# Kernel optimization log

Measured on AMD Instinct MI355X. Metric: run time of the kernel, lower is better.

The kernel has to match this reference:

```python
import jax, jax.numpy as jnp
import numpy as np

B, S, E, L, H, FF, CB = 16, 1000, 512, 4, 8, 2048, 4096
DH = E // H

def _ln(x, g, b):
    m = x.mean(-1, keepdims=True)
    v = ((x - m) ** 2).mean(-1, keepdims=True)
    return (x - m) / jnp.sqrt(v + 1e-5) * g + b

def setup_inputs() -> dict:
    key = jax.random.key(0)
    cnt = [0]
    def rn(shape, s=0.02):
        cnt[0] += 1
        return jax.random.normal(jax.random.fold_in(key, cnt[0]), shape, jnp.float32) * s
    inp = {}
    inp['noisy_tokens'] = jax.random.randint(jax.random.fold_in(key, 999), (B, S), 0, CB, dtype=jnp.int32)
    inp['codebook'] = rn((CB, E), 1.0)
    # sinusoidal positional encoding, as in _create_positional_encoding
    pe = np.zeros((S, E), np.float32)
    pos = np.arange(S, dtype=np.float32)[:, None]
    div = np.exp(np.arange(0, E, 2, dtype=np.float32) * (-np.log(10000.0) / E))
    pe[:, 0::2] = np.sin(pos * div)
    pe[:, 1::2] = np.cos(pos * div)
    inp['pos_enc'] = jnp.asarray(pe)[None]  # [1,S,E]
    # transformer encoder layers (stacked over L)
    inp['qkv_w'] = rn((L, 3 * E, E)); inp['qkv_b'] = jnp.zeros((L, 3 * E))
    inp['out_w'] = rn((L, E, E));     inp['out_b'] = jnp.zeros((L, E))
    inp['ln1_g'] = jnp.ones((L, E));  inp['ln1_b'] = jnp.zeros((L, E))
    inp['ln2_g'] = jnp.ones((L, E));  inp['ln2_b'] = jnp.zeros((L, E))
    inp['ff1_w'] = rn((L, FF, E));    inp['ff1_b'] = jnp.zeros((L, FF))
    inp['ff2_w'] = rn((L, E, FF));    inp['ff2_b'] = jnp.zeros((L, E))
    inp['fin_g'] = jnp.ones((E,));    inp['fin_b'] = jnp.zeros((E,))
    # post_process: Linear, LN, GELU, Linear
    inp['pp1_w'] = rn((E, E)); inp['pp1_b'] = jnp.zeros((E,))
    inp['pp_ln_g'] = jnp.ones((E,)); inp['pp_ln_b'] = jnp.zeros((E,))
    inp['pp2_w'] = rn((E, E)); inp['pp2_b'] = jnp.zeros((E,))
    inp['res_w'] = jnp.float32(0.1)
    # feature_to_codebook: Linear, LN, GELU, Linear (codebook_dim == E)
    inp['fc1_w'] = rn((E, E)); inp['fc1_b'] = jnp.zeros((E,))
    inp['fc_ln_g'] = jnp.ones((E,)); inp['fc_ln_b'] = jnp.zeros((E,))
    inp['fc2_w'] = rn((E, E)); inp['fc2_b'] = jnp.zeros((E,))
    return inp

def reference(noisy_tokens, codebook, pos_enc, qkv_w, qkv_b, out_w, out_b,
              ln1_g, ln1_b, ln2_g, ln2_b, ff1_w, ff1_b, ff2_w, ff2_b,
              fin_g, fin_b, pp1_w, pp1_b, pp_ln_g, pp_ln_b, pp2_w, pp2_b,
              res_w, fc1_w, fc1_b, fc_ln_g, fc_ln_b, fc2_w, fc2_b):
    gelu = lambda z: jax.nn.gelu(z, approximate=False)
    # token embedding (codebook_projection is Identity) + positional encoding
    x = codebook[noisy_tokens] + pos_enc            # [B,S,E]
    # pre-norm transformer encoder (dropout=0 / eval)
    y = x
    for l in range(L):
        h = _ln(y, ln1_g[l], ln1_b[l])
        qkv = h @ qkv_w[l].T + qkv_b[l]             # [B,S,3E]
        q, k, v = jnp.split(qkv, 3, axis=-1)
        q = q.reshape(B, S, H, DH); k = k.reshape(B, S, H, DH); v = v.reshape(B, S, H, DH)
        scores = jnp.einsum('bqhd,bkhd->bhqk', q, k) / jnp.sqrt(jnp.float32(DH))
        attn = jax.nn.softmax(scores, axis=-1)
        ctx = jnp.einsum('bhqk,bkhd->bqhd', attn, v).reshape(B, S, E)
        y = y + (ctx @ out_w[l].T + out_b[l])
        h2 = _ln(y, ln2_g[l], ln2_b[l])
        y = y + (gelu(h2 @ ff1_w[l].T + ff1_b[l]) @ ff2_w[l].T + ff2_b[l])
    y = _ln(y, fin_g, fin_b)
    # post_process + residual
    pp = gelu(_ln(y @ pp1_w.T + pp1_b, pp_ln_g, pp_ln_b)) @ pp2_w.T + pp2_b
    enhanced = x + res_w * pp
    # feature_to_codebook
    fc = gelu(_ln(enhanced @ fc1_w.T + fc1_b, fc_ln_g, fc_ln_b)) @ fc2_w.T + fc2_b  # [B,S,E]
    # quantize: nearest neighbour in codebook (cdist + argmin)
    flat = fc.reshape(-1, E)
    d2 = (jnp.sum(flat ** 2, -1, keepdims=True)
          - 2.0 * flat @ codebook.T
          + jnp.sum(codebook ** 2, -1))            # [B*S, CB]
    tokens = jnp.argmin(d2, axis=-1).reshape(B, S)
    return fc, tokens
```

## Files before the change

### kernel.cpp

```cpp
#include <hip/hip_runtime.h>
#include <hip/hip_bf16.h>
#include <math.h>

#define NTOK 16000
#define E    512
#define FFD  2048
#define CBN  4096
#define SEQ  1000
#define NH   8
#define VLD  1008

typedef __hip_bfloat16 bf16;
typedef __attribute__((ext_vector_type(8))) short short8;
typedef __attribute__((ext_vector_type(4))) float f32x4;

__device__ __forceinline__ float gelu_f(float v) {
    return 0.5f * v * (1.0f + erff(v * 0.70710678118654752f));
}

__device__ __forceinline__ void split_store(float v, bf16* hi, bf16* lo, size_t idx) {
    bf16 h = __float2bfloat16(v);
    hi[idx] = h;
    lo[idx] = __float2bfloat16(v - __bfloat162float(h));
}

__device__ __forceinline__ void gll16(const bf16* g, short* l) {
    __builtin_amdgcn_global_load_lds((const __attribute__((address_space(1))) void*)g,
                                     (__attribute__((address_space(3))) void*)l, 16, 0, 0);
}

__device__ __forceinline__ void t2_ins(float v, int c, float& v1, int& c1, float& v2, int& c2) {
    const bool b1 = (v < v1) || (v == v1 && c < c1);
    const bool b2 = (v < v2) || (v == v2 && c < c2);
    if (b1) { v2 = v1; c2 = c1; v1 = v; c1 = c; }
    else if (b2) { v2 = v; c2 = c; }
}

__global__ __launch_bounds__(128) void embed_kernel(const int* __restrict__ tok,
                                                    const float* __restrict__ cb,
                                                    const float* __restrict__ pe,
                                                    float* __restrict__ y) {
    const int row = blockIdx.x;
    const int s = row % SEQ;
    const int t = tok[row];
    const int c = threadIdx.x * 4;
    const float4 cv = *(const float4*)(cb + (size_t)t * E + c);
    const float4 pv = *(const float4*)(pe + (size_t)s * E + c);
    *(float4*)(y + (size_t)row * E + c) =
        make_float4(cv.x + pv.x, cv.y + pv.y, cv.z + pv.z, cv.w + pv.w);
}

__global__ __launch_bounds__(256) void split_w(const float* __restrict__ src, int ld,
                                               int cols_log2, int n,
                                               bf16* __restrict__ hi, bf16* __restrict__ lo) {
    const int i = blockIdx.x * 256 + threadIdx.x;
    if (i >= n) return;
    const int r = i >> cols_log2;
    const int c = i & ((1 << cols_log2) - 1);
    const float v = src[(size_t)r * ld + c];
    split_store(v, hi, lo, i);
}

template<int GELU>
__global__ __launch_bounds__(256) void ln_planes(const float* __restrict__ in,
                                                 bf16* __restrict__ hi, bf16* __restrict__ lo,
                                                 const float* __restrict__ g,
                                                 const float* __restrict__ b) {
    const int lane = threadIdx.x & 63;
    const int row = blockIdx.x * 4 + (threadIdx.x >> 6);
    const float* p = in + (size_t)row * E;
    const float4 v0 = *(const float4*)(p + lane * 4);
    const float4 v1 = *(const float4*)(p + 256 + lane * 4);
    float sum = v0.x + v0.y + v0.z + v0.w + v1.x + v1.y + v1.z + v1.w;
    float sq = v0.x * v0.x + v0.y * v0.y + v0.z * v0.z + v0.w * v0.w
             + v1.x * v1.x + v1.y * v1.y + v1.z * v1.z + v1.w * v1.w;
#pragma unroll
    for (int m = 1; m < 64; m <<= 1) {
        sum += __shfl_xor(sum, m);
        sq += __shfl_xor(sq, m);
    }
    const float mean = sum * (1.0f / 512.0f);
    const float var = sq * (1.0f / 512.0f) - mean * mean;
    const float rstd = rsqrtf(var + 1e-5f);
    const float4 g0 = *(const float4*)(g + lane * 4);
    const float4 g1 = *(const float4*)(g + 256 + lane * 4);
    const float4 b0 = *(const float4*)(b + lane * 4);
    const float4 b1 = *(const float4*)(b + 256 + lane * 4);
    const size_t base = (size_t)row * E;
    float o;
    const float vv0[4] = {v0.x, v0.y, v0.z, v0.w};
    const float gg0[4] = {g0.x, g0.y, g0.z, g0.w};
    const float bb0[4] = {b0.x, b0.y, b0.z, b0.w};
    const float vv1[4] = {v1.x, v1.y, v1.z, v1.w};
    const float gg1[4] = {g1.x, g1.y, g1.z, g1.w};
    const float bb1[4] = {b1.x, b1.y, b1.z, b1.w};
#pragma unroll
    for (int t = 0; t < 4; ++t) {
        o = (vv0[t] - mean) * rstd * gg0[t] + bb0[t];
        if (GELU) o = gelu_f(o);
        split_store(o, hi, lo, base + lane * 4 + t);
        o = (vv1[t] - mean) * rstd * gg1[t] + bb1[t];
        if (GELU) o = gelu_f(o);
        split_store(o, hi, lo, base + 256 + lane * 4 + t);
    }
}

template<int OUT>
__global__ __launch_bounds__(256) void gemm_split(
    const bf16* __restrict__ Ah, const bf16* __restrict__ Al, int lda,
    const bf16* __restrict__ Wh, const bf16* __restrict__ Wl, int ldw,
    const float* __restrict__ bias,
    float* __restrict__ C, int ldc,
    bf16* __restrict__ Ohi, bf16* __restrict__ Olo, int ldp,
    const int* __restrict__ noisy, const float* __restrict__ cb,
    const float* __restrict__ pe, const float* __restrict__ resw,
    int K) {
    __shared__ __align__(16) short SB[2][4][128][32];
    const int tid = threadIdx.x;
    const int rowBase = blockIdx.y * 128;
    const int colBase = blockIdx.x * 128;
    const int wave = tid >> 6, lane = tid & 63;
    const int wm = (wave & 1) * 64, wn = (wave >> 1) * 64;
    const int lm = lane & 15;
    const int psl8 = ((lane >> 4) ^ ((lm >> 1) & 3)) * 8;

    const bf16* src = (wave == 0) ? Ah : (wave == 1) ? Al : (wave == 2) ? Wh : Wl;
    const int sld = (wave < 2) ? lda : ldw;
    const int srb = (wave < 2) ? rowBase : colBase;
    const int sslot = (lane & 3) ^ ((lane >> 3) & 3);
    const bf16* sp = src + (size_t)(srb + (lane >> 2)) * sld + sslot * 8;
    short* lb0 = &SB[0][wave][0][0];
    short* lb1 = &SB[1][wave][0][0];

    f32x4 acc[4][4];
#pragma unroll
    for (int i = 0; i < 4; ++i)
#pragma unroll
        for (int j = 0; j < 4; ++j)
            acc[i][j] = (f32x4){0.f, 0.f, 0.f, 0.f};

    const int nt = K >> 5;
#pragma unroll
    for (int j = 0; j < 8; ++j)
        gll16(sp + (size_t)j * 16 * sld, lb0 + j * 512);
    {
        const bf16* p = sp + 32;
#pragma unroll
        for (int j = 0; j < 8; ++j)
            gll16(p + (size_t)j * 16 * sld, lb1 + j * 512);
    }
    for (int t = 0; t < nt; ++t) {
        const int cur = t & 1;
        if (t + 1 < nt) asm volatile("s_waitcnt vmcnt(8)" ::: "memory");
        else            asm volatile("s_waitcnt vmcnt(0)" ::: "memory");
        __builtin_amdgcn_s_barrier();
        __builtin_amdgcn_sched_barrier(0);
        const short (*P)[128][32] = SB[cur];
        short8 ah[4], al[4], wh[4], wl[4];
#pragma unroll
        for (int i = 0; i < 4; ++i) {
            ah[i] = *(const short8*)&P[0][wm + i * 16 + lm][psl8];
            al[i] = *(const short8*)&P[1][wm + i * 16 + lm][psl8];
            wh[i] = *(const short8*)&P[2][wn + i * 16 + lm][psl8];
            wl[i] = *(const short8*)&P[3][wn + i * 16 + lm][psl8];
        }
#pragma unroll
        for (int i = 0; i < 4; ++i)
#pragma unroll
            for (int j = 0; j < 4; ++j)
                acc[i][j] = __builtin_amdgcn_mfma_f32_16x16x32_bf16(ah[i], wh[j], acc[i][j], 0, 0, 0);
#pragma unroll
        for (int i = 0; i < 4; ++i)
#pragma unroll
            for (int j = 0; j < 4; ++j)
                acc[i][j] = __builtin_amdgcn_mfma_f32_16x16x32_bf16(ah[i], wl[j], acc[i][j], 0, 0, 0);
#pragma unroll
        for (int i = 0; i < 4; ++i)
#pragma unroll
            for (int j = 0; j < 4; ++j)
                acc[i][j] = __builtin_amdgcn_mfma_f32_16x16x32_bf16(al[i], wh[j], acc[i][j], 0, 0, 0);
        __builtin_amdgcn_s_barrier();
        if (t + 2 < nt) {
            short* lb = cur ? lb1 : lb0;
            const bf16* p = sp + (t + 2) * 32;
#pragma unroll
            for (int j = 0; j < 8; ++j)
                gll16(p + (size_t)j * 16 * sld, lb + j * 512);
        }
    }

    float bv[4];
#pragma unroll
    for (int j = 0; j < 4; ++j)
        bv[j] = bias ? bias[colBase + wn + j * 16 + lm] : 0.f;
    float scv = 0.f;
    if (OUT == 3) scv = resw[0];
#pragma unroll
    for (int i = 0; i < 4; ++i) {
#pragma unroll
        for (int reg = 0; reg < 4; ++reg) {
            const int r = rowBase + wm + i * 16 + (lane >> 4) * 4 + reg;
            int tok = 0, srow = 0;
            if (OUT == 3) { tok = noisy[r]; srow = r % SEQ; }
#pragma unroll
            for (int j = 0; j < 4; ++j) {
                const int col = colBase + wn + j * 16 + lm;
                float v = acc[i][j][reg] + bv[j];
                if (OUT == 0) {
                    C[(size_t)r * ldc + col] = v;
                } else if (OUT == 1) {
                    float* cp = C + (size_t)r * ldc + col;
                    *cp = *cp + v;
                } else if (OUT == 2) {
                    v = gelu_f(v);
                    split_store(v, Ohi, Olo, (size_t)r * ldp + col);
                } else if (OUT == 3) {
                    const float xv = cb[(size_t)tok * E + col] + pe[(size_t)srow * E + col];
                    v = xv + scv * v;
                    split_store(v, Ohi, Olo, (size_t)r * ldp + col);
                } else if (OUT == 4) {
                    split_store(v, Ohi, Olo, (size_t)r * ldp + col);
                } else {
                    C[(size_t)r * ldc + col] = v;
                    split_store(v, Ohi, Olo, (size_t)r * ldp + col);
                }
            }
        }
    }
}

__global__ __launch_bounds__(256) void vtrans(const bf16* __restrict__ vh_src,
                                              const bf16* __restrict__ vl_src,
                                              bf16* __restrict__ vth,
                                              bf16* __restrict__ vtl) {
    __shared__ short T[64][72];
    const int tid = threadIdx.x;
    const int st = blockIdx.x;
    const int bh = blockIdx.y;
    const int b = bh >> 3, h = bh & 7;
    const int sr = tid >> 2, dq = (tid & 3) * 16;
    const int s_g = st * 64 + sr;
    const int od = tid >> 3;
    const int osq = (tid & 7) * 8;
#pragma unroll
    for (int p = 0; p < 2; ++p) {
        const short* src = (const short*)(p ? vl_src : vh_src);
        short* dst = (short*)(p ? vtl : vth);
        short8 a0 = {0, 0, 0, 0, 0, 0, 0, 0};
        short8 a1 = {0, 0, 0, 0, 0, 0, 0, 0};
        if (s_g < SEQ) {
            const short* sp = src + (size_t)(b * SEQ + s_g) * 1536 + 1024 + h * 64 + dq;
            a0 = *(const short8*)sp;
            a1 = *(const short8*)(sp + 8);
        }
        __syncthreads();
#pragma unroll
        for (int j = 0; j < 8; ++j) T[dq + j][sr] = a0[j];
#pragma unroll
        for (int j = 0; j < 8; ++j) T[dq + 8 + j][sr] = a1[j];
        __syncthreads();
        const int scol = st * 64 + osq;
        if (scol + 8 <= VLD) {
            const short8 o0 = *(const short8*)&T[od][osq];
            const short8 o1 = *(const short8*)&T[od + 32][osq];
            *(short8*)(dst + (size_t)(bh * 64 + od) * VLD + scol) = o0;
            *(short8*)(dst + (size_t)(bh * 64 + od + 32) * VLD + scol) = o1;
        }
    }
}

__global__ __launch_bounds__(256) void attn_mfma(const bf16* __restrict__ qkh,
                                                 const bf16* __restrict__ qkl,
                                                 const bf16* __restrict__ vth,
                                                 const bf16* __restrict__ vtl,
                                                 bf16* __restrict__ chi,
                                                 bf16* __restrict__ clo) {
    __shared__ short QPs[2][64][72];
    __shared__ short Ks[2][64][72];
    __shared__ short Vs[2][64][72];
    const int tid = threadIdx.x;
    const int qt = blockIdx.x, bh = blockIdx.y;
    const int b = bh >> 3, h = bh & 7;
    const int wave = tid >> 6, lane = tid & 63;
    const int lm = lane & 15, g = lane >> 4, q8 = g * 8;
    const int wq = wave * 16;
    const int r0 = tid >> 2, kq = (tid & 3) * 16;
    const short8 z = {0, 0, 0, 0, 0, 0, 0, 0};

    {
        const int q = qt * 64 + r0;
        short8 a0 = z, a1 = z, b0 = z, b1 = z;
        if (q < SEQ) {
            const size_t base = (size_t)(b * SEQ + q) * 1536 + h * 64 + kq;
            a0 = *(const short8*)((const short*)qkh + base);
            a1 = *(const short8*)((const short*)qkh + base + 8);
            b0 = *(const short8*)((const short*)qkl + base);
            b1 = *(const short8*)((const short*)qkl + base + 8);
        }
        *(short8*)&QPs[0][r0][kq] = a0; *(short8*)&QPs[0][r0][kq + 8] = a1;
        *(short8*)&QPs[1][r0][kq] = b0; *(short8*)&QPs[1][r0][kq + 8] = b1;
    }
    __syncthreads();
    short8 qfh[2], qfl[2];
#pragma unroll
    for (int t = 0; t < 2; ++t) {
        qfh[t] = *(const short8*)&QPs[0][wq + lm][t * 32 + q8];
        qfl[t] = *(const short8*)&QPs[1][wq + lm][t * 32 + q8];
    }

    float m_i[4] = {-3e38f, -3e38f, -3e38f, -3e38f};
    float l_i[4] = {0.f, 0.f, 0.f, 0.f};
    f32x4 o[4];
#pragma unroll
    for (int dt = 0; dt < 4; ++dt) o[dt] = (f32x4){0.f, 0.f, 0.f, 0.f};

    short8 ka0 = z, ka1 = z, kl0 = z, kl1 = z;
    short8 va0 = z, va1 = z, vl0 = z, vl1 = z;
    auto loadKV = [&](int kb2) {
        const int kr = kb2 + r0;
        ka0 = z; ka1 = z; kl0 = z; kl1 = z;
        if (kr < SEQ) {
            const size_t base = (size_t)(b * SEQ + kr) * 1536 + 512 + h * 64 + kq;
            ka0 = *(const short8*)((const short*)qkh + base);
            ka1 = *(const short8*)((const short*)qkh + base + 8);
            kl0 = *(const short8*)((const short*)qkl + base);
            kl1 = *(const short8*)((const short*)qkl + base + 8);
        }
        const size_t vbase = (size_t)(bh * 64 + r0) * VLD + kb2 + kq;
        va0 = z; va1 = z; vl0 = z; vl1 = z;
        if (kb2 + kq + 8 <= VLD) {
            va0 = *(const short8*)((const short*)vth + vbase);
            vl0 = *(const short8*)((const short*)vtl + vbase);
        }
        if (kb2 + kq + 16 <= VLD) {
            va1 = *(const short8*)((const short*)vth + vbase + 8);
            vl1 = *(const short8*)((const short*)vtl + vbase + 8);
        }
    };
    loadKV(0);

    for (int kb = 0; kb < SEQ; kb += 64) {
        __syncthreads();
        {
            *(short8*)&Ks[0][r0][kq] = ka0; *(short8*)&Ks[0][r0][kq + 8] = ka1;
            *(short8*)&Ks[1][r0][kq] = kl0; *(short8*)&Ks[1][r0][kq + 8] = kl1;
            *(short8*)&Vs[0][r0][kq] = va0; *(short8*)&Vs[0][r0][kq + 8] = va1;
            *(short8*)&Vs[1][r0][kq] = vl0; *(short8*)&Vs[1][r0][kq + 8] = vl1;
        }
        __syncthreads();
        if (kb + 64 < SEQ) loadKV(kb + 64);
        f32x4 sac[4];
#pragma unroll
        for (int j = 0; j < 4; ++j) sac[j] = (f32x4){0.f, 0.f, 0.f, 0.f};
#pragma unroll
        for (int t = 0; t < 2; ++t) {
#pragma unroll
            for (int j = 0; j < 4; ++j) {
                const short8 kh = *(const short8*)&Ks[0][j * 16 + lm][t * 32 + q8];
                const short8 kl = *(const short8*)&Ks[1][j * 16 + lm][t * 32 + q8];
                sac[j] = __builtin_amdgcn_mfma_f32_16x16x32_bf16(qfh[t], kh, sac[j], 0, 0, 0);
                sac[j] = __builtin_amdgcn_mfma_f32_16x16x32_bf16(qfh[t], kl, sac[j], 0, 0, 0);
                sac[j] = __builtin_amdgcn_mfma_f32_16x16x32_bf16(qfl[t], kh, sac[j], 0, 0, 0);
            }
        }
        float alpha_v[4];
#pragma unroll
        for (int reg = 0; reg < 4; ++reg) {
            float sv[4];
            float rm = -3e38f;
#pragma unroll
            for (int j = 0; j < 4; ++j) {
                const int kc = kb + j * 16 + lm;
                float s = sac[j][reg] * 0.125f;
                s = (kc < SEQ) ? s : -3e38f;
                sv[j] = s;
                rm = fmaxf(rm, s);
            }
#pragma unroll
            for (int m = 1; m < 16; m <<= 1) rm = fmaxf(rm, __shfl_xor(rm, m));
            const float mn = fmaxf(m_i[reg], rm);
            const float al = expf(m_i[reg] - mn);
            float rs = 0.f;
            const int prow = wq + g * 4 + reg;
#pragma unroll
            for (int j = 0; j < 4; ++j) {
                const float pv = expf(sv[j] - mn);
                rs += pv;
                bf16 phb = __float2bfloat16(pv);
                bf16 plb = __float2bfloat16(pv - __bfloat162float(phb));
                QPs[0][prow][j * 16 + lm] = *reinterpret_cast<short*>(&phb);
                QPs[1][prow][j * 16 + lm] = *reinterpret_cast<short*>(&plb);
            }
#pragma unroll
            for (int m = 1; m < 16; m <<= 1) rs += __shfl_xor(rs, m);
            l_i[reg] = l_i[reg] * al + rs;
            m_i[reg] = mn;
            alpha_v[reg] = al;
        }
        const f32x4 av = {alpha_v[0], alpha_v[1], alpha_v[2], alpha_v[3]};
#pragma unroll
        for (int dt = 0; dt < 4; ++dt) o[dt] *= av;
        __syncthreads();
#pragma unroll
        for (int t = 0; t < 2; ++t) {
            const short8 ph = *(const short8*)&QPs[0][wq + lm][t * 32 + q8];
            const short8 pl = *(const short8*)&QPs[1][wq + lm][t * 32 + q8];
#pragma unroll
            for (int dt = 0; dt < 4; ++dt) {
                const short8 vh = *(const short8*)&Vs[0][dt * 16 + lm][t * 32 + q8];
                const short8 vl = *(const short8*)&Vs[1][dt * 16 + lm][t * 32 + q8];
                o[dt] = __builtin_amdgcn_mfma_f32_16x16x32_bf16(ph, vh, o[dt], 0, 0, 0);
                o[dt] = __builtin_amdgcn_mfma_f32_16x16x32_bf16(ph, vl, o[dt], 0, 0, 0);
                o[dt] = __builtin_amdgcn_mfma_f32_16x16x32_bf16(pl, vh, o[dt], 0, 0, 0);
            }
        }
    }
#pragma unroll
    for (int reg = 0; reg < 4; ++reg) {
        const int q = qt * 64 + wq + g * 4 + reg;
        if (q < SEQ) {
            const float inv = 1.0f / l_i[reg];
#pragma unroll
            for (int dt = 0; dt < 4; ++dt) {
                const size_t idx = (size_t)(b * SEQ + q) * E + h * 64 + dt * 16 + lm;
                split_store(o[dt][reg] * inv, chi, clo, idx);
            }
        }
    }
}

__global__ __launch_bounds__(256) void cbnorm_kernel(const float* __restrict__ cb,
                                                     float* __restrict__ out) {
    const int lane = threadIdx.x & 63;
    const int row = blockIdx.x * 4 + (threadIdx.x >> 6);
    const float* p = cb + (size_t)row * E;
    const float4 v0 = *(const float4*)(p + lane * 4);
    const float4 v1 = *(const float4*)(p + 256 + lane * 4);
    float sq = v0.x * v0.x + v0.y * v0.y + v0.z * v0.z + v0.w * v0.w
             + v1.x * v1.x + v1.y * v1.y + v1.z * v1.z + v1.w * v1.w;
#pragma unroll
    for (int m = 1; m < 64; m <<= 1) sq += __shfl_xor(sq, m);
    if (lane == 0) out[row] = sq;
}

__global__ __launch_bounds__(256) void argmin_mfma(
    const bf16* __restrict__ Ah, const bf16* __restrict__ Al,
    const bf16* __restrict__ Wh, const bf16* __restrict__ Wl,
    const float* __restrict__ cbn, float4* __restrict__ part) {
    __shared__ __align__(16) short SB[2][4][128][32];
    float4* mrg = reinterpret_cast<float4*>(&SB[0][0][0][0]);
    const int tid = threadIdx.x;
    const int rowBase = blockIdx.y * 128;
    const int wave = tid >> 6, lane = tid & 63;
    const int wm = wave * 32;
    const int lm = lane & 15;
    const int g = lane >> 4;
    const int psl8 = (g ^ ((lm >> 1) & 3)) * 8;
    const int own_row = tid >> 1;
    const int own_half = tid & 1;

    const bf16* ssrc = (wave == 0) ? Ah : (wave == 1) ? Al : (wave == 2) ? Wh : Wl;
    const int sslot = (lane & 3) ^ ((lane >> 3) & 3);
    short* lb0 = &SB[0][wave][0][0];
    short* lb1 = &SB[1][wave][0][0];

    float rv1 = 3e38f, rv2 = 3e38f;
    int rc1 = 0x7fffffff, rc2 = 0x7fffffff;

    for (int ct = 0; ct < 4; ++ct) {
        const int colBase = blockIdx.x * 512 + ct * 128;
        const int rb = (wave < 2) ? rowBase : colBase;
        const bf16* sp = ssrc + (size_t)(rb + (lane >> 2)) * E + sslot * 8;
        f32x4 acc[2][8];
#pragma unroll
        for (int i = 0; i < 2; ++i)
#pragma unroll
            for (int j = 0; j < 8; ++j)
                acc[i][j] = (f32x4){0.f, 0.f, 0.f, 0.f};

        __builtin_amdgcn_s_barrier();
#pragma unroll
        for (int j = 0; j < 8; ++j)
            gll16(sp + (size_t)j * 16 * E, lb0 + j * 512);
        {
            const bf16* p = sp + 32;
#pragma unroll
            for (int j = 0; j < 8; ++j)
                gll16(p + (size_t)j * 16 * E, lb1 + j * 512);
        }
        for (int t = 0; t < 16; ++t) {
            const int cur = t & 1;
            if (t < 15) asm volatile("s_waitcnt vmcnt(8)" ::: "memory");
            else        asm volatile("s_waitcnt vmcnt(0)" ::: "memory");
            __builtin_amdgcn_s_barrier();
            __builtin_amdgcn_sched_barrier(0);
            const short (*P)[128][32] = SB[cur];
            short8 ah[2], al2[2], wh[8], wl[8];
#pragma unroll
            for (int i = 0; i < 2; ++i) {
                ah[i]  = *(const short8*)&P[0][wm + i * 16 + lm][psl8];
                al2[i] = *(const short8*)&P[1][wm + i * 16 + lm][psl8];
            }
#pragma unroll
            for (int j = 0; j < 8; ++j) {
                wh[j] = *(const short8*)&P[2][j * 16 + lm][psl8];
                wl[j] = *(const short8*)&P[3][j * 16 + lm][psl8];
            }
#pragma unroll
            for (int i = 0; i < 2; ++i)
#pragma unroll
                for (int j = 0; j < 8; ++j)
                    acc[i][j] = __builtin_amdgcn_mfma_f32_16x16x32_bf16(ah[i], wh[j], acc[i][j], 0, 0, 0);
#pragma unroll
            for (int i = 0; i < 2; ++i)
#pragma unroll
                for (int j = 0; j < 8; ++j)
                    acc[i][j] = __builtin_amdgcn_mfma_f32_16x16x32_bf16(ah[i], wl[j], acc[i][j], 0, 0, 0);
#pragma unroll
            for (int i = 0; i < 2; ++i)
#pragma unroll
                for (int j = 0; j < 8; ++j)
                    acc[i][j] = __builtin_amdgcn_mfma_f32_16x16x32_bf16(al2[i], wh[j], acc[i][j], 0, 0, 0);
            __builtin_amdgcn_s_barrier();
            if (t < 14) {
                short* lb = cur ? lb1 : lb0;
                const bf16* p = sp + (t + 2) * 32;
#pragma unroll
                for (int j = 0; j < 8; ++j)
                    gll16(p + (size_t)j * 16 * E, lb + j * 512);
            }
        }

        float nv[8];
#pragma unroll
        for (int j = 0; j < 8; ++j) nv[j] = cbn[colBase + j * 16 + lm];
#pragma unroll
        for (int i = 0; i < 2; ++i) {
#pragma unroll
            for (int reg = 0; reg < 4; ++reg) {
                const int row_local = wm + i * 16 + g * 4 + reg;
                float v1 = 3e38f, v2 = 3e38f;
                int c1 = 0x7fffffff, c2 = 0x7fffffff;
#pragma unroll
                for (int j = 0; j < 8; ++j) {
                    const float d = nv[j] - 2.0f * acc[i][j][reg];
                    t2_ins(d, colBase + j * 16 + lm, v1, c1, v2, c2);
                }
                mrg[row_local * 16 + (lm ^ (row_local & 15))] = make_float4(v1, (float)c1, v2, (float)c2);
            }
        }
        __syncthreads();
        {
            float mv1 = 3e38f, mv2 = 3e38f;
            int mc1 = 0x7fffffff, mc2 = 0x7fffffff;
#pragma unroll
            for (int e = 0; e < 8; ++e) {
                const int cc = own_half * 8 + e;
                const float4 p = mrg[own_row * 16 + (cc ^ (own_row & 15))];
                t2_ins(p.x, (int)p.y, mv1, mc1, mv2, mc2);
                t2_ins(p.z, (int)p.w, mv1, mc1, mv2, mc2);
            }
            const float pv1 = __shfl_xor(mv1, 1); const int pc1 = __shfl_xor(mc1, 1);
            const float pv2 = __shfl_xor(mv2, 1); const int pc2 = __shfl_xor(mc2, 1);
            t2_ins(pv1, pc1, mv1, mc1, mv2, mc2);
            t2_ins(pv2, pc2, mv1, mc1, mv2, mc2);
            t2_ins(mv1, mc1, rv1, rc1, rv2, rc2);
            t2_ins(mv2, mc2, rv1, rc1, rv2, rc2);
        }
    }
    if (own_half == 0)
        part[(size_t)(rowBase + own_row) * 8 + blockIdx.x] =
            make_float4(rv1, (float)rc1, rv2, (float)rc2);
}

__global__ __launch_bounds__(256) void argmin_exact(const float4* __restrict__ part,
                                                    const float* __restrict__ fc,
                                                    const float* __restrict__ cb,
                                                    const float* __restrict__ cbn,
                                                    float* __restrict__ tokf) {
    const int wave = threadIdx.x >> 6, lane = threadIdx.x & 63;
    const int r = blockIdx.x * 4 + wave;
    float v1 = 3e38f, v2 = 3e38f;
    int c1 = 0x7fffffff, c2 = 0x7fffffff;
    if (lane < 8) {
        const float4 p = part[(size_t)r * 8 + lane];
        v1 = p.x; c1 = (int)p.y; v2 = p.z; c2 = (int)p.w;
    }
#pragma unroll
    for (int m = 1; m < 8; m <<= 1) {
        const float w1 = __shfl_xor(v1, m); const int d1i = __shfl_xor(c1, m);
        const float w2 = __shfl_xor(v2, m); const int d2i = __shfl_xor(c2, m);
        t2_ins(w1, d1i, v1, c1, v2, c2);
        t2_ins(w2, d2i, v1, c1, v2, c2);
    }
    c1 = __shfl(c1, 0);
    c2 = __shfl(c2, 0);
    const float* fr = fc + (size_t)r * E + lane * 8;
    const float* p1 = cb + (size_t)c1 * E + lane * 8;
    const float* p2 = cb + (size_t)c2 * E + lane * 8;
    float d1 = 0.f, d2 = 0.f;
#pragma unroll
    for (int j = 0; j < 8; ++j) {
        const float f = fr[j];
        d1 += f * p1[j];
        d2 += f * p2[j];
    }
#pragma unroll
    for (int m = 1; m < 64; m <<= 1) {
        d1 += __shfl_xor(d1, m);
        d2 += __shfl_xor(d2, m);
    }
    d1 = cbn[c1] - 2.0f * d1;
    d2 = cbn[c2] - 2.0f * d2;
    const int win = ((d1 < d2) || (d1 == d2 && c1 < c2)) ? c1 : c2;
    if (lane == 0) tokf[r] = (float)win;
}

extern "C" void kernel_launch(void* const* d_in, const int* in_sizes, int n_in,
                              void* d_out, int out_size, void* d_ws, size_t ws_size,
                              hipStream_t stream) {
    const int* noisy = (const int*)d_in[0];
    const float* codebook = (const float*)d_in[1];
    const float* pos_enc = (const float*)d_in[2];
    const float* qkv_w = (const float*)d_in[3];
    const float* qkv_b = (const float*)d_in[4];
    const float* out_w = (const float*)d_in[5];
    const float* out_b = (const float*)d_in[6];
    const float* ln1_g = (const float*)d_in[7];
    const float* ln1_b = (const float*)d_in[8];
    const float* ln2_g = (const float*)d_in[9];
    const float* ln2_b = (const float*)d_in[10];
    const float* ff1_w = (const float*)d_in[11];
    const float* ff1_b = (const float*)d_in[12];
    const float* ff2_w = (const float*)d_in[13];
    const float* ff2_b = (const float*)d_in[14];
    const float* fin_g = (const float*)d_in[15];
    const float* fin_b = (const float*)d_in[16];
    const float* pp1_w = (const float*)d_in[17];
    const float* pp1_b = (const float*)d_in[18];
    const float* pp_ln_g = (const float*)d_in[19];
    const float* pp_ln_b = (const float*)d_in[20];
    const float* pp2_w = (const float*)d_in[21];
    const float* pp2_b = (const float*)d_in[22];
    const float* res_w = (const float*)d_in[23];
    const float* fc1_w = (const float*)d_in[24];
    const float* fc1_b = (const float*)d_in[25];
    const float* fc_ln_g = (const float*)d_in[26];
    const float* fc_ln_b = (const float*)d_in[27];
    const float* fc2_w = (const float*)d_in[28];
    const float* fc2_b = (const float*)d_in[29];

    float* ws = (float*)d_ws;
    float* y = ws;
    float* REG = ws + 8192000;
    bf16* qkvh = (bf16*)REG;
    bf16* qkvl = qkvh + 24576000;
    bf16* mid_hi = (bf16*)REG;
    bf16* mid_lo = mid_hi + 16384000;
    float* slotA = REG;
    float* slotB = REG + 8192000;
    bf16* e_hi = (bf16*)slotA;
    bf16* e_lo = e_hi + 8192000;
    bf16* fcp2_hi = (bf16*)(REG + 16384000);
    bf16* fcp2_lo = fcp2_hi + 8192000;
    float* WV = ws + 32768000;
    bf16* vth = (bf16*)WV;
    bf16* vtl = vth + 8192 * VLD;
    bf16* wA_hi = (bf16*)WV;
    bf16* wA_lo = wA_hi + 1048576;
    bf16* wB_hi = wA_lo + 1048576;
    bf16* wB_lo = wB_hi + 1048576;
    bf16* cbh = wB_lo + 1048576;
    bf16* cbl = cbh + 2097152;
    float* cbn = slotB;
    float4* part = (float4*)(slotB + 4096);
    bf16* h_hi = (bf16*)d_out;
    bf16* h_lo = h_hi + 8192000;
    float* tokf = (float*)d_out + 8192000;

    const dim3 blk(256);
    const dim3 g512(4, 125), g1024(8, 125), g1536(12, 125);

    embed_kernel<<<dim3(NTOK), dim3(128), 0, stream>>>(noisy, codebook, pos_enc, y);

    for (int l = 0; l < 4; ++l) {
        ln_planes<0><<<dim3(4000), blk, 0, stream>>>(y, h_hi, h_lo, ln1_g + l * E, ln1_b + l * E);
        split_w<<<dim3(3072), blk, 0, stream>>>(qkv_w + (size_t)l * 1536 * E, E, 9, 1536 * E, wA_hi, wA_lo);
        gemm_split<4><<<g1536, blk, 0, stream>>>(
            h_hi, h_lo, E, wA_hi, wA_lo, E, qkv_b + (size_t)l * 1536,
            nullptr, 0, qkvh, qkvl, 1536, nullptr, nullptr, nullptr, nullptr, E);
        vtrans<<<dim3(16, 128), blk, 0, stream>>>(qkvh, qkvl, vth, vtl);
        attn_mfma<<<dim3(16, 128), blk, 0, stream>>>(qkvh, qkvl, vth, vtl, h_hi, h_lo);
        split_w<<<dim3(1024), blk, 0, stream>>>(out_w + (size_t)l * E * E, E, 9, E * E, wB_hi, wB_lo);
        gemm_split<1><<<g512, blk, 0, stream>>>(
            h_hi, h_lo, E, wB_hi, wB_lo, E, out_b + (size_t)l * E,
            y, E, nullptr, nullptr, 0, nullptr, nullptr, nullptr, nullptr, E);
        ln_planes<0><<<dim3(4000), blk, 0, stream>>>(y, h_hi, h_lo, ln2_g + l * E, ln2_b + l * E);
        split_w<<<dim3(4096), blk, 0, stream>>>(ff1_w + (size_t)l * FFD * E, E, 9, FFD * E, wA_hi, wA_lo);
        split_w<<<dim3(4096), blk, 0, stream>>>(ff2_w + (size_t)l * E * FFD, FFD, 11, E * FFD, wB_hi, wB_lo);
        for (int c = 0; c < 2; ++c) {
            gemm_split<2><<<g1024, blk, 0, stream>>>(
                h_hi, h_lo, E, wA_hi + (size_t)c * 1024 * E, wA_lo + (size_t)c * 1024 * E, E,
                ff1_b + (size_t)l * FFD + c * 1024,
                nullptr, 0, mid_hi, mid_lo, 1024, nullptr, nullptr, nullptr, nullptr, E);
            gemm_split<1><<<g512, blk, 0, stream>>>(
                mid_hi, mid_lo, 1024, wB_hi + c * 1024, wB_lo + c * 1024, FFD,
                (c == 0) ? (ff2_b + (size_t)l * E) : nullptr,
                y, E, nullptr, nullptr, 0, nullptr, nullptr, nullptr, nullptr, 1024);
        }
    }

    ln_planes<0><<<dim3(4000), blk, 0, stream>>>(y, h_hi, h_lo, fin_g, fin_b);
    split_w<<<dim3(1024), blk, 0, stream>>>(pp1_w, E, 9, E * E, wA_hi, wA_lo);
    gemm_split<0><<<g512, blk, 0, stream>>>(
        h_hi, h_lo, E, wA_hi, wA_lo, E, pp1_b,
        slotB, E, nullptr, nullptr, 0, nullptr, nullptr, nullptr, nullptr, E);
    ln_planes<1><<<dim3(4000), blk, 0, stream>>>(slotB, h_hi, h_lo, pp_ln_g, pp_ln_b);
    split_w<<<dim3(1024), blk, 0, stream>>>(pp2_w, E, 9, E * E, wB_hi, wB_lo);
    gemm_split<3><<<g512, blk, 0, stream>>>(
        h_hi, h_lo, E, wB_hi, wB_lo, E, pp2_b,
        nullptr, 0, e_hi, e_lo, E, noisy, codebook, pos_enc, res_w, E);
    split_w<<<dim3(1024), blk, 0, stream>>>(fc1_w, E, 9, E * E, wA_hi, wA_lo);
    gemm_split<0><<<g512, blk, 0, stream>>>(
        e_hi, e_lo, E, wA_hi, wA_lo, E, fc1_b,
        slotB, E, nullptr, nullptr, 0, nullptr, nullptr, nullptr, nullptr, E);
    ln_planes<1><<<dim3(4000), blk, 0, stream>>>(slotB, h_hi, h_lo, fc_ln_g, fc_ln_b);
    split_w<<<dim3(1024), blk, 0, stream>>>(fc2_w, E, 9, E * E, wB_hi, wB_lo);
    gemm_split<5><<<g512, blk, 0, stream>>>(
        h_hi, h_lo, E, wB_hi, wB_lo, E, fc2_b,
        slotA, E, fcp2_hi, fcp2_lo, E, nullptr, nullptr, nullptr, nullptr, E);

    split_w<<<dim3(8192), blk, 0, stream>>>(codebook, E, 9, CBN * E, cbh, cbl);
    cbnorm_kernel<<<dim3(1024), blk, 0, stream>>>(codebook, cbn);
    argmin_mfma<<<dim3(8, 125), blk, 0, stream>>>(fcp2_hi, fcp2_lo, cbh, cbl, cbn, part);
    argmin_exact<<<dim3(4000), blk, 0, stream>>>(part, slotA, codebook, cbn, tokf);
    hipMemcpyAsync(d_out, slotA, (size_t)8192000 * 4, hipMemcpyDeviceToDevice, stream);
}
```

Before: 3.503 ms.

## Keep fc operand in registers and stream full codebook per block in argmin

Restructures the MFMA nearest-neighbour kernel so each block owns 64 rows, keeps the row operand hi/lo planes in registers, and streams all codebook tiles through double-buffered LDS. Top-2 candidates are tracked in registers across all columns and reduced with shuffles, which removes the per-tile LDS merge and the 8-way partial merge in the exact-rescoring kernel. The cost is a much smaller grid with one block per CU and high register pressure, which may reduce latency hiding.

```diff
diff --git a/kernel.cpp b/kernel.cpp
--- a/kernel.cpp
+++ b/kernel.cpp
@@ -443,134 +443,106 @@
     if (lane == 0) out[row] = sq;
 }
 
-__global__ __launch_bounds__(256) void argmin_mfma(
+__global__ __launch_bounds__(256, 1) void argmin_mfma(
     const bf16* __restrict__ Ah, const bf16* __restrict__ Al,
     const bf16* __restrict__ Wh, const bf16* __restrict__ Wl,
     const float* __restrict__ cbn, float4* __restrict__ part) {
-    __shared__ __align__(16) short SB[2][4][128][32];
-    float4* mrg = reinterpret_cast<float4*>(&SB[0][0][0][0]);
+    __shared__ __align__(16) short Wreg[2][8192];
     const int tid = threadIdx.x;
-    const int rowBase = blockIdx.y * 128;
+    const int rowBase = blockIdx.x * 64;
     const int wave = tid >> 6, lane = tid & 63;
-    const int wm = wave * 32;
-    const int lm = lane & 15;
-    const int g = lane >> 4;
+    const int lm = lane & 15, g = lane >> 4;
+    const int g8 = g * 8;
     const int psl8 = (g ^ ((lm >> 1) & 3)) * 8;
-    const int own_row = tid >> 1;
-    const int own_half = tid & 1;
-
-    const bf16* ssrc = (wave == 0) ? Ah : (wave == 1) ? Al : (wave == 2) ? Wh : Wl;
     const int sslot = (lane & 3) ^ ((lane >> 3) & 3);
-    short* lb0 = &SB[0][wave][0][0];
-    short* lb1 = &SB[1][wave][0][0];
-
-    float rv1 = 3e38f, rv2 = 3e38f;
-    int rc1 = 0x7fffffff, rc2 = 0x7fffffff;
-
-    for (int ct = 0; ct < 4; ++ct) {
-        const int colBase = blockIdx.x * 512 + ct * 128;
-        const int rb = (wave < 2) ? rowBase : colBase;
-        const bf16* sp = ssrc + (size_t)(rb + (lane >> 2)) * E + sslot * 8;
-        f32x4 acc[2][8];
-#pragma unroll
-        for (int i = 0; i < 2; ++i)
-#pragma unroll
-            for (int j = 0; j < 8; ++j)
-                acc[i][j] = (f32x4){0.f, 0.f, 0.f, 0.f};
-
-        __builtin_amdgcn_s_barrier();
-#pragma unroll
-        for (int j = 0; j < 8; ++j)
-            gll16(sp + (size_t)j * 16 * E, lb0 + j * 512);
-        {
-            const bf16* p = sp + 32;
-#pragma unroll
-            for (int j = 0; j < 8; ++j)
-                gll16(p + (size_t)j * 16 * E, lb1 + j * 512);
-        }
-        for (int t = 0; t < 16; ++t) {
-            const int cur = t & 1;
-            if (t < 15) asm volatile("s_waitcnt vmcnt(8)" ::: "memory");
-            else        asm volatile("s_waitcnt vmcnt(0)" ::: "memory");
+    const int srow = lane >> 2;
+    const int row = rowBase + wave * 16 + lm;
+
+    short8 a_h[16], a_l[16];
+#pragma unroll
+    for (int c = 0; c < 16; ++c) {
+        a_h[c] = *(const short8*)(Ah + (size_t)row * E + c * 32 + g8);
+        a_l[c] = *(const short8*)(Al + (size_t)row * E + c * 32 + g8);
+    }
+
+    auto stageW = [&](int s) {
+        const int ct = s >> 4, k = s & 15;
+        const int colB = ct * 128;
+        short* dstb = &Wreg[s & 1][0];
+#pragma unroll
+        for (int e = 0; e < 4; ++e) {
+            const int m = wave * 4 + e;
+            const int p = m >> 3;
+            const int j = m & 7;
+            const bf16* srcp = p ? Wl : Wh;
+            gll16(srcp + (size_t)(colB + j * 16 + srow) * E + k * 32 + sslot * 8,
+                  dstb + ((p * 128 + j * 16) * 32));
+        }
+    };
+    stageW(0);
+    stageW(1);
+
+    float rv1[4], rv2[4];
+    int rc1[4], rc2[4];
+#pragma unroll
+    for (int r = 0; r < 4; ++r) {
+        rv1[r] = 3e38f; rv2[r] = 3e38f;
+        rc1[r] = 0x7fffffff; rc2[r] = 0x7fffffff;
+    }
+    f32x4 acc[8];
+#pragma unroll
+    for (int j = 0; j < 8; ++j) acc[j] = (f32x4){0.f, 0.f, 0.f, 0.f};
+
+    for (int ct = 0; ct < 32; ++ct) {
+        const int colB = ct * 128;
+#pragma unroll
+        for (int k = 0; k < 16; ++k) {
+            const int s = ct * 16 + k;
+            if (s + 1 < 512) asm volatile("s_waitcnt vmcnt(4)" ::: "memory");
+            else             asm volatile("s_waitcnt vmcnt(0)" ::: "memory");
             __builtin_amdgcn_s_barrier();
             __builtin_amdgcn_sched_barrier(0);
-            const short (*P)[128][32] = SB[cur];
-            short8 ah[2], al2[2], wh[8], wl[8];
-#pragma unroll
-            for (int i = 0; i < 2; ++i) {
-                ah[i]  = *(const short8*)&P[0][wm + i * 16 + lm][psl8];
-                al2[i] = *(const short8*)&P[1][wm + i * 16 + lm][psl8];
-            }
+            const short* B = &Wreg[s & 1][0];
 #pragma unroll
             for (int j = 0; j < 8; ++j) {
-                wh[j] = *(const short8*)&P[2][j * 16 + lm][psl8];
-                wl[j] = *(const short8*)&P[3][j * 16 + lm][psl8];
-            }
-#pragma unroll
-            for (int i = 0; i < 2; ++i)
-#pragma unroll
-                for (int j = 0; j < 8; ++j)
-                    acc[i][j] = __builtin_amdgcn_mfma_f32_16x16x32_bf16(ah[i], wh[j], acc[i][j], 0, 0, 0);
-#pragma unroll
-            for (int i = 0; i < 2; ++i)
-#pragma unroll
-                for (int j = 0; j < 8; ++j)
-                    acc[i][j] = __builtin_amdgcn_mfma_f32_16x16x32_bf16(ah[i], wl[j], acc[i][j], 0, 0, 0);
-#pragma unroll
-            for (int i = 0; i < 2; ++i)
-#pragma unroll
-                for (int j = 0; j < 8; ++j)
-                    acc[i][j] = __builtin_amdgcn_mfma_f32_16x16x32_bf16(al2[i], wh[j], acc[i][j], 0, 0, 0);
+                const short8 wh = *(const short8*)(B + (j * 16 + lm) * 32 + psl8);
+                const short8 wl = *(const short8*)(B + (128 + j * 16 + lm) * 32 + psl8);
+                acc[j] = __builtin_amdgcn_mfma_f32_16x16x32_bf16(a_h[k], wh, acc[j], 0, 0, 0);
+                acc[j] = __builtin_amdgcn_mfma_f32_16x16x32_bf16(a_h[k], wl, acc[j], 0, 0, 0);
+                acc[j] = __builtin_amdgcn_mfma_f32_16x16x32_bf16(a_l[k], wh, acc[j], 0, 0, 0);
+            }
             __builtin_amdgcn_s_barrier();
-            if (t < 14) {
-                short* lb = cur ? lb1 : lb0;
-                const bf16* p = sp + (t + 2) * 32;
-#pragma unroll
-                for (int j = 0; j < 8; ++j)
-                    gll16(p + (size_t)j * 16 * E, lb + j * 512);
-            }
-        }
-
-        float nv[8];
-#pragma unroll
-        for (int j = 0; j < 8; ++j) nv[j] = cbn[colBase + j * 16 + lm];
-#pragma unroll
-        for (int i = 0; i < 2; ++i) {
-#pragma unroll
-            for (int reg = 0; reg < 4; ++reg) {
-                const int row_local = wm + i * 16 + g * 4 + reg;
-                float v1 = 3e38f, v2 = 3e38f;
-                int c1 = 0x7fffffff, c2 = 0x7fffffff;
-#pragma unroll
-                for (int j = 0; j < 8; ++j) {
-                    const float d = nv[j] - 2.0f * acc[i][j][reg];
-                    t2_ins(d, colBase + j * 16 + lm, v1, c1, v2, c2);
-                }
-                mrg[row_local * 16 + (lm ^ (row_local & 15))] = make_float4(v1, (float)c1, v2, (float)c2);
-            }
-        }
-        __syncthreads();
-        {
-            float mv1 = 3e38f, mv2 = 3e38f;
-            int mc1 = 0x7fffffff, mc2 = 0x7fffffff;
-#pragma unroll
-            for (int e = 0; e < 8; ++e) {
-                const int cc = own_half * 8 + e;
-                const float4 p = mrg[own_row * 16 + (cc ^ (own_row & 15))];
-                t2_ins(p.x, (int)p.y, mv1, mc1, mv2, mc2);
-                t2_ins(p.z, (int)p.w, mv1, mc1, mv2, mc2);
-            }
-            const float pv1 = __shfl_xor(mv1, 1); const int pc1 = __shfl_xor(mc1, 1);
-            const float pv2 = __shfl_xor(mv2, 1); const int pc2 = __shfl_xor(mc2, 1);
-            t2_ins(pv1, pc1, mv1, mc1, mv2, mc2);
-            t2_ins(pv2, pc2, mv1, mc1, mv2, mc2);
-            t2_ins(mv1, mc1, rv1, rc1, rv2, rc2);
-            t2_ins(mv2, mc2, rv1, rc1, rv2, rc2);
-        }
-    }
-    if (own_half == 0)
-        part[(size_t)(rowBase + own_row) * 8 + blockIdx.x] =
-            make_float4(rv1, (float)rc1, rv2, (float)rc2);
+            if (s + 2 < 512) stageW(s + 2);
+        }
+#pragma unroll
+        for (int j = 0; j < 8; ++j) {
+            const int col = colB + j * 16 + lm;
+            const float nv = cbn[col];
+#pragma unroll
+            for (int r = 0; r < 4; ++r) {
+                const float d = nv - 2.0f * acc[j][r];
+                t2_ins(d, col, rv1[r], rc1[r], rv2[r], rc2[r]);
+            }
+            acc[j] = (f32x4){0.f, 0.f, 0.f, 0.f};
+        }
+    }
+
+#pragma unroll
+    for (int r = 0; r < 4; ++r) {
+#pragma unroll
+        for (int m = 1; m < 16; m <<= 1) {
+            const float w1 = __shfl_xor(rv1[r], m); const int d1 = __shfl_xor(rc1[r], m);
+            const float w2 = __shfl_xor(rv2[r], m); const int d2 = __shfl_xor(rc2[r], m);
+            t2_ins(w1, d1, rv1[r], rc1[r], rv2[r], rc2[r]);
+            t2_ins(w2, d2, rv1[r], rc1[r], rv2[r], rc2[r]);
+        }
+    }
+    if (lm == 0) {
+#pragma unroll
+        for (int r = 0; r < 4; ++r)
+            part[rowBase + wave * 16 + g * 4 + r] =
+                make_float4(rv1[r], (float)rc1[r], rv2[r], (float)rc2[r]);
+    }
 }
 
 __global__ __launch_bounds__(256) void argmin_exact(const float4* __restrict__ part,
@@ -580,21 +552,9 @@
                                                     float* __restrict__ tokf) {
     const int wave = threadIdx.x >> 6, lane = threadIdx.x & 63;
     const int r = blockIdx.x * 4 + wave;
-    float v1 = 3e38f, v2 = 3e38f;
-    int c1 = 0x7fffffff, c2 = 0x7fffffff;
-    if (lane < 8) {
-        const float4 p = part[(size_t)r * 8 + lane];
-        v1 = p.x; c1 = (int)p.y; v2 = p.z; c2 = (int)p.w;
-    }
-#pragma unroll
-    for (int m = 1; m < 8; m <<= 1) {
-        const float w1 = __shfl_xor(v1, m); const int d1i = __shfl_xor(c1, m);
-        const float w2 = __shfl_xor(v2, m); const int d2i = __shfl_xor(c2, m);
-        t2_ins(w1, d1i, v1, c1, v2, c2);
-        t2_ins(w2, d2i, v1, c1, v2, c2);
-    }
-    c1 = __shfl(c1, 0);
-    c2 = __shfl(c2, 0);
+    const float4 p = part[r];
+    const int c1 = (int)p.y;
+    const int c2 = (int)p.w;
     const float* fr = fc + (size_t)r * E + lane * 8;
     const float* p1 = cb + (size_t)c1 * E + lane * 8;
     const float* p2 = cb + (size_t)c2 * E + lane * 8;
@@ -732,7 +692,7 @@
 
     split_w<<<dim3(8192), blk, 0, stream>>>(codebook, E, 9, CBN * E, cbh, cbl);
     cbnorm_kernel<<<dim3(1024), blk, 0, stream>>>(codebook, cbn);
-    argmin_mfma<<<dim3(8, 125), blk, 0, stream>>>(fcp2_hi, fcp2_lo, cbh, cbl, cbn, part);
+    argmin_mfma<<<dim3(250), blk, 0, stream>>>(fcp2_hi, fcp2_lo, cbh, cbl, cbn, part);
     argmin_exact<<<dim3(4000), blk, 0, stream>>>(part, slotA, codebook, cbn, tokf);
     hipMemcpyAsync(d_out, slotA, (size_t)8192000 * 4, hipMemcpyDeviceToDevice, stream);
 }
```

After: 3.663 ms. 1.05x slower.
